# Optimization experiments

Measured on AMD Instinct MI355X. Metric: run time of the kernel, lower is better.

Reference implementation:

```python
import jax, jax.numpy as jnp
import numpy as np

B, H, W, C = 8, 64, 64, 768
NH, HD = 12, 64          # heads, head_dim
WS = 14                  # window size
MLP = 3072
EPS = 1e-6
SCALE = HD ** -0.5


def _layernorm(x, g, b):
    mu = jnp.mean(x, -1, keepdims=True)
    var = jnp.mean(jnp.square(x - mu), -1, keepdims=True)
    return (x - mu) * jax.lax.rsqrt(var + EPS) * g + b


def setup_inputs() -> dict:
    key = jax.random.key(0)
    ks = jax.random.split(key, 16)
    s = 0.02
    return {
        "hidden_states": jax.random.normal(ks[0], (B, H, W, C), jnp.float32),
        "ln1_g": jnp.ones((C,), jnp.float32),
        "ln1_b": jnp.zeros((C,), jnp.float32),
        "qkv_w": jax.random.normal(ks[1], (C, 3 * C), jnp.float32) * s,  # (in, out)
        "qkv_b": jnp.zeros((3 * C,), jnp.float32),
        "proj_w": jax.random.normal(ks[2], (C, C), jnp.float32) * s,
        "proj_b": jnp.zeros((C,), jnp.float32),
        "rel_pos_h": jax.random.normal(ks[3], (2 * WS - 1, HD), jnp.float32) * s,
        "rel_pos_w": jax.random.normal(ks[4], (2 * WS - 1, HD), jnp.float32) * s,
        "ln2_g": jnp.ones((C,), jnp.float32),
        "ln2_b": jnp.zeros((C,), jnp.float32),
        "lin1_w": jax.random.normal(ks[5], (C, MLP), jnp.float32) * s,
        "lin1_b": jnp.zeros((MLP,), jnp.float32),
        "lin2_w": jax.random.normal(ks[6], (MLP, C), jnp.float32) * s,
        "lin2_b": jnp.zeros((C,), jnp.float32),
    }


def _attention(x, qkv_w, qkv_b, proj_w, proj_b, rel_pos_h, rel_pos_w):
    # x: (Bw, WS, WS, C) windows
    Bw = x.shape[0]
    N = WS * WS
    qkv = (x.reshape(Bw, N, C) @ qkv_w + qkv_b)              # (Bw, N, 3C)
    qkv = qkv.reshape(Bw, N, 3, NH, HD).transpose(2, 0, 3, 1, 4)
    qkv = qkv.reshape(3, Bw * NH, N, HD)
    q, k, v = qkv[0], qkv[1], qkv[2]
    attn = jnp.einsum('bqd,bkd->bqk', q * SCALE, k)          # (Bw*NH, N, N)
    # decomposed relative position bias (q_size == k_size == WS, no interpolation)
    coords = jnp.arange(WS)[:, None] - jnp.arange(WS)[None, :] + (WS - 1)  # (WS, WS)
    Rh = rel_pos_h[coords]                                    # (WS, WS, HD)
    Rw = rel_pos_w[coords]
    r_q = q.reshape(Bw * NH, WS, WS, HD)
    rel_h = jnp.einsum('bhwc,hkc->bhwk', r_q, Rh)
    rel_w = jnp.einsum('bhwc,wkc->bhwk', r_q, Rw)
    attn = attn.reshape(Bw * NH, WS, WS, WS, WS)
    attn = attn + rel_h[:, :, :, :, None] + rel_w[:, :, :, None, :]
    attn = attn.reshape(Bw * NH, N, N)
    attn = jax.nn.softmax(attn.astype(jnp.float32), axis=-1).astype(q.dtype)
    out = jnp.einsum('bqk,bkd->bqd', attn, v)                 # (Bw*NH, N, HD)
    out = out.reshape(Bw, NH, WS, WS, HD).transpose(0, 2, 3, 1, 4).reshape(Bw, WS, WS, C)
    return out @ proj_w + proj_b


def _layer(x, p):
    residual = x
    h = _layernorm(x, p['ln1_g'], p['ln1_b'])
    # window partition with padding 64 -> 70
    pad_h = (WS - H % WS) % WS
    pad_w = (WS - W % WS) % WS
    h = jnp.pad(h, ((0, 0), (0, pad_h), (0, pad_w), (0, 0)))
    Hp, Wp = H + pad_h, W + pad_w
    nh, nw = Hp // WS, Wp // WS
    h = h.reshape(B, nh, WS, nw, WS, C).transpose(0, 1, 3, 2, 4, 5).reshape(-1, WS, WS, C)
    h = _attention(h, p['qkv_w'], p['qkv_b'], p['proj_w'], p['proj_b'],
                   p['rel_pos_h'], p['rel_pos_w'])
    # unpartition + crop
    h = h.reshape(B, nh, nw, WS, WS, C).transpose(0, 1, 3, 2, 4, 5).reshape(B, Hp, Wp, C)
    h = h[:, :H, :W, :]
    h = residual + h
    ln2 = _layernorm(h, p['ln2_g'], p['ln2_b'])
    mlp = jax.nn.gelu(ln2 @ p['lin1_w'] + p['lin1_b'], approximate=False) @ p['lin2_w'] + p['lin2_b']
    return h + mlp


def reference(hidden_states, ln1_g, ln1_b, qkv_w, qkv_b, proj_w, proj_b,
              rel_pos_h, rel_pos_w, ln2_g, ln2_b, lin1_w, lin1_b, lin2_w, lin2_b):
    p = dict(ln1_g=ln1_g, ln1_b=ln1_b, qkv_w=qkv_w, qkv_b=qkv_b,
             proj_w=proj_w, proj_b=proj_b, rel_pos_h=rel_pos_h, rel_pos_w=rel_pos_w,
             ln2_g=ln2_g, ln2_b=ln2_b, lin1_w=lin1_w, lin1_b=lin1_b,
             lin2_w=lin2_w, lin2_b=lin2_b)
    return _layer(hidden_states, p)
```

## Files before the change

### kernel.cpp

```cpp
#include <hip/hip_runtime.h>
#include <hip/hip_bf16.h>
#include <math.h>
#include <stdint.h>

typedef unsigned short u16;
typedef __attribute__((ext_vector_type(8))) short bf16x8;
typedef __attribute__((ext_vector_type(4))) float f32x4;

__device__ __forceinline__ float b2f(u16 u) {
  union { float f; uint32_t i; } v; v.i = ((uint32_t)u) << 16; return v.f;
}
__device__ __forceinline__ u16 f2b(float f) {
  union { float f; uint32_t i; } v; v.f = f;
  uint32_t x = v.i;
  return (u16)((x + 0x7fffu + ((x >> 16) & 1u)) >> 16);
}

__device__ __forceinline__ void gl_lds16(const u16* g, u16* l) {
  __builtin_amdgcn_global_load_lds(
      (const __attribute__((address_space(1))) void*)g,
      (__attribute__((address_space(3))) void*)l, 16, 0, 0);
}

__global__ __launch_bounds__(256)
void transpose_w(const float* __restrict__ in, u16* __restrict__ out, int K, int N) {
  __shared__ float t[32][33];
  const int x = threadIdx.x & 31;
  const int y = threadIdx.x >> 5;
  const int n0 = blockIdx.x * 32;
  const int k0 = blockIdx.y * 32;
  #pragma unroll
  for (int yy = 0; yy < 32; yy += 8)
    t[y + yy][x] = in[(size_t)(k0 + y + yy) * N + n0 + x];
  __syncthreads();
  #pragma unroll
  for (int yy = 0; yy < 32; yy += 8)
    out[(size_t)(n0 + y + yy) * K + k0 + x] = f2b(t[x][y + yy]);
}

__global__ __launch_bounds__(256)
void rel_cast(const float* __restrict__ rph, const float* __restrict__ rpw,
              u16* __restrict__ RHB, u16* __restrict__ RWB)
{
  const int i = blockIdx.x * 256 + threadIdx.x;
  if (i < 27 * 64) { RHB[i] = f2b(rph[i]); RWB[i] = f2b(rpw[i]); }
}

__global__ __launch_bounds__(256)
void ln_f32(const float* __restrict__ xin, const float* __restrict__ g,
            const float* __restrict__ b, u16* __restrict__ out)
{
  const int R = blockIdx.x * 4 + (threadIdx.x >> 6);
  const int lane = threadIdx.x & 63;
  const float* p = xin + (size_t)R * 768 + lane * 12;
  float v[12];
  float4 a0 = *(const float4*)(p);
  float4 a1 = *(const float4*)(p + 4);
  float4 a2 = *(const float4*)(p + 8);
  v[0]=a0.x; v[1]=a0.y; v[2]=a0.z;  v[3]=a0.w;
  v[4]=a1.x; v[5]=a1.y; v[6]=a1.z;  v[7]=a1.w;
  v[8]=a2.x; v[9]=a2.y; v[10]=a2.z; v[11]=a2.w;
  float sum = 0.f, sq = 0.f;
  #pragma unroll
  for (int i = 0; i < 12; ++i) { sum += v[i]; sq += v[i] * v[i]; }
  #pragma unroll
  for (int m = 1; m < 64; m <<= 1) { sum += __shfl_xor(sum, m); sq += __shfl_xor(sq, m); }
  const float mu  = sum * (1.0f / 768.0f);
  const float var = sq * (1.0f / 768.0f) - mu * mu;
  const float rs  = rsqrtf(var + 1e-6f);
  u16 o[12];
  #pragma unroll
  for (int i = 0; i < 12; ++i)
    o[i] = f2b((v[i] - mu) * rs * g[lane * 12 + i] + b[lane * 12 + i]);
  u16* q = out + (size_t)R * 768 + lane * 12;
  *(ushort4*)(q)     = make_ushort4(o[0], o[1], o[2],  o[3]);
  *(ushort4*)(q + 4) = make_ushort4(o[4], o[5], o[6],  o[7]);
  *(ushort4*)(q + 8) = make_ushort4(o[8], o[9], o[10], o[11]);
}

__global__ __launch_bounds__(256)
void qkv_padfill(const float* __restrict__ qkv_b,
                 u16* __restrict__ Qb, u16* __restrict__ Kb, u16* __restrict__ Vtb)
{
  const int R = blockIdx.x * 4 + (threadIdx.x >> 6);
  const int lane = threadIdx.x & 63;
  const int win = R / 196, n = R - win * 196;
  const int r25 = win % 25;
  const int wh = r25 / 5, ww = r25 - wh * 5;
  const int ii = n / 14,  jj = n - ii * 14;
  const int gh = wh * 14 + ii, gw = ww * 14 + jj;
  if (gh < 64 && gw < 64) return;
  #pragma unroll
  for (int head = 0; head < 12; ++head) {
    const size_t bh = (size_t)(win * 12 + head);
    Qb[(bh * 196 + n) * 64 + lane]  = f2b(qkv_b[head * 64 + lane]);
    Kb[(bh * 196 + n) * 64 + lane]  = f2b(qkv_b[768 + head * 64 + lane] * 0.125f);
    Vtb[(bh * 64 + lane) * 224 + n] = f2b(qkv_b[1536 + head * 64 + lane]);
  }
}

template<int EPI>
__global__ __launch_bounds__(256)
void gemm_bt(const u16* __restrict__ A, const u16* __restrict__ BT,
             int M, int N, int K,
             const float* __restrict__ bias,
             void* __restrict__ out0, u16* __restrict__ out1, u16* __restrict__ out2,
             const float* __restrict__ extra)
{
  __shared__ __align__(16) u16 As[128 * 32];
  __shared__ __align__(16) u16 Bs[128 * 32];
  const int tid  = threadIdx.x;
  const int lane = tid & 63;
  const int wave = tid >> 6;
  const int m0 = blockIdx.x * 128;
  const int n0 = blockIdx.y * 128;
  const int wm = (wave >> 1) << 6;
  const int wn = (wave & 1) << 6;
  const int cl = lane & 15;
  const int q4 = lane >> 4;

  f32x4 acc[4][4];
  #pragma unroll
  for (int i = 0; i < 4; ++i)
    #pragma unroll
    for (int j = 0; j < 4; ++j) acc[i][j] = f32x4{0.f, 0.f, 0.f, 0.f};

  const int sr = tid >> 2;
  const int sk = (tid & 3) << 3;
  const u16* ag0 = A  + (size_t)(m0 + sr) * K + sk;
  const u16* ag1 = A  + (size_t)(m0 + 64 + sr) * K + sk;
  const u16* bg0 = BT + (size_t)(n0 + sr) * K + sk;
  const u16* bg1 = BT + (size_t)(n0 + 64 + sr) * K + sk;

  for (int k0 = 0; k0 < K; k0 += 32) {
    __syncthreads();
    gl_lds16(ag0 + k0, &As[tid * 8]);
    gl_lds16(ag1 + k0, &As[tid * 8 + 2048]);
    gl_lds16(bg0 + k0, &Bs[tid * 8]);
    gl_lds16(bg1 + k0, &Bs[tid * 8 + 2048]);
    __syncthreads();
    bf16x8 af[4], bfv[4];
    #pragma unroll
    for (int i = 0; i < 4; ++i) af[i]  = *(const bf16x8*)&As[(wm + i * 16 + cl) * 32 + q4 * 8];
    #pragma unroll
    for (int i = 0; i < 4; ++i) bfv[i] = *(const bf16x8*)&Bs[(wn + i * 16 + cl) * 32 + q4 * 8];
    #pragma unroll
    for (int i = 0; i < 4; ++i)
      #pragma unroll
      for (int j = 0; j < 4; ++j)
        acc[i][j] = __builtin_amdgcn_mfma_f32_16x16x32_bf16(af[i], bfv[j], acc[i][j], 0, 0, 0);
  }

  #pragma unroll
  for (int mt = 0; mt < 4; ++mt) {
    #pragma unroll
    for (int nt = 0; nt < 4; ++nt) {
      const int gcol = n0 + wn + nt * 16 + cl;
      const float bval = bias[gcol];
      #pragma unroll
      for (int i = 0; i < 4; ++i) {
        const int grow = m0 + wm + mt * 16 + q4 * 4 + i;
        if (grow >= M) continue;
        float v = acc[mt][nt][i] + bval;
        if (EPI == 0) {
          const int bb = grow >> 12, rem = grow & 4095;
          const int gh = rem >> 6, gw = rem & 63;
          const int wh = gh / 14, ii = gh - wh * 14;
          const int ww = gw / 14, jj = gw - ww * 14;
          const int win = bb * 25 + wh * 5 + ww;
          const int n = ii * 14 + jj;
          const int s = (gcol >= 1536) ? 2 : (gcol >= 768 ? 1 : 0);
          const int rem2 = gcol - s * 768;
          const int head = rem2 >> 6, hd = rem2 & 63;
          const size_t bh = (size_t)(win * 12 + head);
          if (s == 0)      ((u16*)out0)[(bh * 196 + n) * 64 + hd] = f2b(v);
          else if (s == 1) out1[(bh * 196 + n) * 64 + hd] = f2b(v * 0.125f);
          else             out2[(bh * 64 + hd) * 224 + n] = f2b(v);
        } else if (EPI == 1) {
          const size_t idx = (size_t)grow * 768 + gcol;
          ((float*)out0)[idx] = v + extra[idx];
        } else {
          const float u2 = v * (1.5957691216f + 0.0713548163f * v * v);
          const float gl = v / (1.0f + __expf(-u2));
          ((u16*)out0)[(size_t)grow * 3072 + gcol] = f2b(gl);
        }
      }
    }
  }
}

__global__ __launch_bounds__(256)
void attn_kernel(const u16* __restrict__ Qb, const u16* __restrict__ Kb,
                 const u16* __restrict__ Vtb,
                 const u16* __restrict__ RHB, const u16* __restrict__ RWB,
                 u16* __restrict__ outO)
{
  __shared__ __align__(16) float Ss[32 * 201];
  __shared__ u16 MhAll[196 * 14];
  __shared__ u16 MwAll[196 * 14];
  __shared__ float Sinv[32];
  u16* Ps = (u16*)Ss;

  const int tid  = threadIdx.x;
  const int lane = tid & 63;
  const int wave = tid >> 6;
  const int cl = lane & 15;
  const int q4 = lane >> 4;
  const int bh = blockIdx.x;
  const int win = bh / 12, head = bh - win * 12;
  const int bb = win / 25, r25 = win - bb * 25;
  const int wwh = r25 / 5, www = r25 - wwh * 5;

  const u16* Qbh = Qb  + (size_t)bh * 196 * 64;
  const u16* Kbh = Kb  + (size_t)bh * 196 * 64;
  const u16* Vbh = Vtb + (size_t)bh * 64 * 224;

  for (int t = wave; t < 28; t += 4) {
    const int isW = t >= 14;
    const int grp = isW ? t - 14 : t;
    const int qrow = isW ? cl * 14 + grp : grp * 14 + cl;
    int trow = grp - cl + 13; trow = trow < 0 ? 0 : trow;
    const u16* TB = isW ? RWB : RHB;
    f32x4 acc = f32x4{0.f, 0.f, 0.f, 0.f};
    #pragma unroll
    for (int ks = 0; ks < 2; ++ks) {
      bf16x8 a  = *(const bf16x8*)(Qbh + (size_t)qrow * 64 + ks * 32 + q4 * 8);
      bf16x8 bv = *(const bf16x8*)(TB + (size_t)trow * 64 + ks * 32 + q4 * 8);
      acc = __builtin_amdgcn_mfma_f32_16x16x32_bf16(a, bv, acc, 0, 0, 0);
    }
    if (cl < 14) {
      #pragma unroll
      for (int i = 0; i < 4; ++i) {
        const int r = q4 * 4 + i;
        if (r < 14) {
          if (isW) MwAll[(r * 14 + grp) * 14 + cl] = f2b(acc[i]);
          else     MhAll[(grp * 14 + r) * 14 + cl] = f2b(acc[i]);
        }
      }
    }
  }
  __syncthreads();

  for (int c = 0; c < 7; ++c) {
    const int qbase = c * 32;
    bf16x8 afr[2][2];
    #pragma unroll
    for (int mt = 0; mt < 2; ++mt)
      #pragma unroll
      for (int ks = 0; ks < 2; ++ks)
        afr[mt][ks] = *(const bf16x8*)(Qbh + (size_t)(qbase + mt * 16 + cl) * 64 + ks * 32 + q4 * 8);

    for (int t = wave; t < 26; t += 4) {
      const int mt = t / 13, nt = t - mt * 13;
      const int col = nt * 16 + cl;
      f32x4 acc = f32x4{0.f, 0.f, 0.f, 0.f};
      #pragma unroll
      for (int ks = 0; ks < 2; ++ks) {
        bf16x8 bv = *(const bf16x8*)(Kbh + (size_t)col * 64 + ks * 32 + q4 * 8);
        acc = __builtin_amdgcn_mfma_f32_16x16x32_bf16(afr[mt][ks], bv, acc, 0, 0, 0);
      }
      if (col < 196) {
        const int kh = col / 14, kw = col - kh * 14;
        #pragma unroll
        for (int i = 0; i < 4; ++i) {
          const int r = mt * 16 + q4 * 4 + i;
          const int gq = qbase + r;
          float bias = 0.f;
          if (gq < 196) bias = b2f(MhAll[gq * 14 + kh]) + b2f(MwAll[gq * 14 + kw]);
          Ss[r * 201 + col] = acc[i] + bias;
        }
      }
    }
    __syncthreads();

    const int r = wave * 8 + (lane >> 3);
    const int s = lane & 7;
    float e[25];
    float sum = 0.f;
    #pragma unroll
    for (int k = 0; k < 25; ++k) {
      const int col = s + 8 * k;
      float ex = 0.f;
      if (col < 196) ex = __expf(fminf(Ss[r * 201 + col], 60.f));
      e[k] = ex;
      sum += ex;
    }
    sum += __shfl_xor(sum, 1);
    sum += __shfl_xor(sum, 2);
    sum += __shfl_xor(sum, 4);
    if (s == 0) Sinv[r] = 1.0f / sum;
    __syncthreads();

    #pragma unroll
    for (int k = 0; k < 25; ++k) {
      const int col = s + 8 * k;
      Ps[r * 232 + col] = (col < 196) ? f2b(e[k]) : (u16)0;
    }
    for (int z = tid; z < 384; z += 256) {
      const int rr = z / 12, m = z - rr * 12;
      *(uint32_t*)&Ps[rr * 232 + 200 + 2 * m] = 0;
    }
    __syncthreads();

    {
      const int hd = wave * 16 + cl;
      f32x4 acc0 = f32x4{0.f, 0.f, 0.f, 0.f};
      f32x4 acc1 = f32x4{0.f, 0.f, 0.f, 0.f};
      #pragma unroll
      for (int ks = 0; ks < 7; ++ks) {
        bf16x8 bv = *(const bf16x8*)(Vbh + (size_t)hd * 224 + ks * 32 + q4 * 8);
        bf16x8 a0 = *(const bf16x8*)&Ps[(cl)      * 232 + ks * 32 + q4 * 8];
        bf16x8 a1 = *(const bf16x8*)&Ps[(16 + cl) * 232 + ks * 32 + q4 * 8];
        acc0 = __builtin_amdgcn_mfma_f32_16x16x32_bf16(a0, bv, acc0, 0, 0, 0);
        acc1 = __builtin_amdgcn_mfma_f32_16x16x32_bf16(a1, bv, acc1, 0, 0, 0);
      }
      #pragma unroll
      for (int i = 0; i < 4; ++i) {
        #pragma unroll
        for (int half = 0; half < 2; ++half) {
          const int q = qbase + half * 16 + q4 * 4 + i;
          if (q < 196) {
            const float av = (half ? acc1[i] : acc0[i]) * Sinv[half * 16 + q4 * 4 + i];
            const int ii = q / 14, jj = q - ii * 14;
            const int gh = wwh * 14 + ii, gw = www * 14 + jj;
            if (gh < 64 && gw < 64)
              outO[(((size_t)bb * 64 + gh) * 64 + gw) * 768 + head * 64 + hd] = f2b(av);
          }
        }
      }
    }
    __syncthreads();
  }
}

extern "C" void kernel_launch(void* const* d_in, const int* in_sizes, int n_in,
                              void* d_out, int out_size, void* d_ws, size_t ws_size,
                              hipStream_t stream)
{
  (void)in_sizes; (void)n_in; (void)out_size; (void)ws_size;
  const float* x      = (const float*)d_in[0];
  const float* ln1_g  = (const float*)d_in[1];
  const float* ln1_b  = (const float*)d_in[2];
  const float* qkv_w  = (const float*)d_in[3];
  const float* qkv_b  = (const float*)d_in[4];
  const float* proj_w = (const float*)d_in[5];
  const float* proj_b = (const float*)d_in[6];
  const float* rph    = (const float*)d_in[7];
  const float* rpw    = (const float*)d_in[8];
  const float* ln2_g  = (const float*)d_in[9];
  const float* ln2_b  = (const float*)d_in[10];
  const float* lin1_w = (const float*)d_in[11];
  const float* lin1_b = (const float*)d_in[12];
  const float* lin2_w = (const float*)d_in[13];
  const float* lin2_b = (const float*)d_in[14];
  float* outF = (float*)d_out;

  char* ws = (char*)d_ws;
  size_t off = 0;
  auto allocB = [&](size_t bytes) -> char* {
    char* p = ws + off;
    off += (bytes + 255) & ~(size_t)255;
    return p;
  };
  u16* qkvT  = (u16*)allocB((size_t)2304 * 768 * 2);
  u16* projT = (u16*)allocB((size_t)768 * 768 * 2);
  u16* lin1T = (u16*)allocB((size_t)3072 * 768 * 2);
  u16* lin2T = (u16*)allocB((size_t)768 * 3072 * 2);
  u16* RHB   = (u16*)allocB((size_t)(27 * 64 + 64) * 2);
  u16* RWB   = (u16*)allocB((size_t)(27 * 64 + 64) * 2);
  u16* xn    = (u16*)allocB((size_t)32768 * 768 * 2);
  char* region = allocB((size_t)189235200);
  u16* Qb   = (u16*)region;
  u16* Kb   = Qb + (size_t)30105600;
  u16* Vtb  = Kb + (size_t)30105600;
  float* hbuf = (float*)region;
  u16* midQ = (u16*)(region + (size_t)100663296);

  dim3 blk(256);
  transpose_w<<<dim3(72, 24), blk, 0, stream>>>(qkv_w,  qkvT, 768, 2304);
  transpose_w<<<dim3(24, 24), blk, 0, stream>>>(proj_w, projT, 768, 768);
  transpose_w<<<dim3(96, 24), blk, 0, stream>>>(lin1_w, lin1T, 768, 3072);
  transpose_w<<<dim3(24, 96), blk, 0, stream>>>(lin2_w, lin2T, 3072, 768);
  rel_cast<<<7, blk, 0, stream>>>(rph, rpw, RHB, RWB);

  ln_f32<<<8192, blk, 0, stream>>>(x, ln1_g, ln1_b, xn);

  gemm_bt<0><<<dim3(256, 18), blk, 0, stream>>>(xn, qkvT, 32768, 2304, 768,
                                                qkv_b, Qb, Kb, Vtb, nullptr);
  qkv_padfill<<<9800, blk, 0, stream>>>(qkv_b, Qb, Kb, Vtb);

  attn_kernel<<<2400, blk, 0, stream>>>(Qb, Kb, Vtb, RHB, RWB, xn);

  gemm_bt<1><<<dim3(256, 6), blk, 0, stream>>>(xn, projT, 32768, 768, 768,
                                               proj_b, hbuf, nullptr, nullptr, x);

  ln_f32<<<8192, blk, 0, stream>>>(hbuf, ln2_g, ln2_b, xn);

  for (int pass = 0; pass < 4; ++pass) {
    const size_t ro = (size_t)pass * 8192;
    gemm_bt<2><<<dim3(64, 24), blk, 0, stream>>>(xn + ro * 768, lin1T, 8192, 3072, 768,
                                                 lin1_b, midQ, nullptr, nullptr, nullptr);
    gemm_bt<1><<<dim3(64, 6), blk, 0, stream>>>(midQ, lin2T, 8192, 768, 3072,
                                                lin2_b, outF + ro * 768, nullptr, nullptr,
                                                hbuf + ro * 768);
  }
}
```

Before: 1.564 ms.

## Remap GEMM workgroups across XCDs, use nontemporal epilogue stores, halve MLP passes

Remaps the linear workgroup id so consecutive tiles are grouped per chiplet (stride by 8). This is meant to improve L2 reuse of shared A/B tiles on the multi-XCD MI355X. The epilogue hoists the window/row index math out of the column loop and uses nontemporal loads and stores for outputs and the residual. The MLP now runs in 2 passes of 16384 rows instead of 4 of 8192, which needs a larger workspace region for the intermediate buffer and cuts the number of launches. The M bound check is dropped, which is safe only because M is a multiple of 128.

After: 1.920 ms. +22.8%, slower.

```diff
diff --git a/kernel.cpp b/kernel.cpp
--- a/kernel.cpp
+++ b/kernel.cpp
@@ -112,8 +112,15 @@
   const int tid  = threadIdx.x;
   const int lane = tid & 63;
   const int wave = tid >> 6;
-  const int m0 = blockIdx.x * 128;
-  const int n0 = blockIdx.y * 128;
+
+  const int nwg = gridDim.x * gridDim.y;
+  const int lid = blockIdx.y * gridDim.x + blockIdx.x;
+  const int nl  = (lid & 7) * (nwg >> 3) + (lid >> 3);
+  const int bx  = nl / gridDim.y;
+  const int by  = nl - bx * gridDim.y;
+  const int m0 = bx * 128;
+  const int n0 = by * 128;
+
   const int wm = (wave >> 1) << 6;
   const int wn = (wave & 1) << 6;
   const int cl = lane & 15;
@@ -153,36 +160,54 @@
 
   #pragma unroll
   for (int mt = 0; mt < 4; ++mt) {
+    int rowW[4], rowN[4];
+    if (EPI == 0) {
+      #pragma unroll
+      for (int i = 0; i < 4; ++i) {
+        const int grow = m0 + wm + mt * 16 + q4 * 4 + i;
+        const int bb = grow >> 12, rem = grow & 4095;
+        const int gh = rem >> 6, gw = rem & 63;
+        const int wh = gh / 14, ii = gh - wh * 14;
+        const int ww = gw / 14, jj = gw - ww * 14;
+        rowW[i] = (bb * 25 + wh * 5 + ww) * 12;
+        rowN[i] = ii * 14 + jj;
+      }
+    }
     #pragma unroll
     for (int nt = 0; nt < 4; ++nt) {
       const int gcol = n0 + wn + nt * 16 + cl;
       const float bval = bias[gcol];
-      #pragma unroll
-      for (int i = 0; i < 4; ++i) {
-        const int grow = m0 + wm + mt * 16 + q4 * 4 + i;
-        if (grow >= M) continue;
-        float v = acc[mt][nt][i] + bval;
-        if (EPI == 0) {
-          const int bb = grow >> 12, rem = grow & 4095;
-          const int gh = rem >> 6, gw = rem & 63;
-          const int wh = gh / 14, ii = gh - wh * 14;
-          const int ww = gw / 14, jj = gw - ww * 14;
-          const int win = bb * 25 + wh * 5 + ww;
-          const int n = ii * 14 + jj;
-          const int s = (gcol >= 1536) ? 2 : (gcol >= 768 ? 1 : 0);
-          const int rem2 = gcol - s * 768;
-          const int head = rem2 >> 6, hd = rem2 & 63;
-          const size_t bh = (size_t)(win * 12 + head);
-          if (s == 0)      ((u16*)out0)[(bh * 196 + n) * 64 + hd] = f2b(v);
-          else if (s == 1) out1[(bh * 196 + n) * 64 + hd] = f2b(v * 0.125f);
-          else             out2[(bh * 64 + hd) * 224 + n] = f2b(v);
-        } else if (EPI == 1) {
+      if (EPI == 0) {
+        const int s = (gcol >= 1536) ? 2 : (gcol >= 768 ? 1 : 0);
+        const int rem2 = gcol - s * 768;
+        const int head = rem2 >> 6, hd = rem2 & 63;
+        #pragma unroll
+        for (int i = 0; i < 4; ++i) {
+          const float v = acc[mt][nt][i] + bval;
+          const size_t bh = (size_t)(rowW[i] + head);
+          if (s == 0)
+            __builtin_nontemporal_store(f2b(v), &((u16*)out0)[(bh * 196 + rowN[i]) * 64 + hd]);
+          else if (s == 1)
+            __builtin_nontemporal_store(f2b(v * 0.125f), &out1[(bh * 196 + rowN[i]) * 64 + hd]);
+          else
+            __builtin_nontemporal_store(f2b(v), &out2[(bh * 64 + hd) * 224 + rowN[i]]);
+        }
+      } else if (EPI == 1) {
+        #pragma unroll
+        for (int i = 0; i < 4; ++i) {
+          const int grow = m0 + wm + mt * 16 + q4 * 4 + i;
           const size_t idx = (size_t)grow * 768 + gcol;
-          ((float*)out0)[idx] = v + extra[idx];
-        } else {
+          const float v = acc[mt][nt][i] + bval + __builtin_nontemporal_load(&extra[idx]);
+          __builtin_nontemporal_store(v, &((float*)out0)[idx]);
+        }
+      } else {
+        #pragma unroll
+        for (int i = 0; i < 4; ++i) {
+          const int grow = m0 + wm + mt * 16 + q4 * 4 + i;
+          const float v = acc[mt][nt][i] + bval;
           const float u2 = v * (1.5957691216f + 0.0713548163f * v * v);
           const float gl = v / (1.0f + __expf(-u2));
-          ((u16*)out0)[(size_t)grow * 3072 + gcol] = f2b(gl);
+          __builtin_nontemporal_store(f2b(gl), &((u16*)out0)[(size_t)grow * 3072 + gcol]);
         }
       }
     }
@@ -369,7 +394,7 @@
   u16* RHB   = (u16*)allocB((size_t)(27 * 64 + 64) * 2);
   u16* RWB   = (u16*)allocB((size_t)(27 * 64 + 64) * 2);
   u16* xn    = (u16*)allocB((size_t)32768 * 768 * 2);
-  char* region = allocB((size_t)189235200);
+  char* region = allocB((size_t)201326592);
   u16* Qb   = (u16*)region;
   u16* Kb   = Qb + (size_t)30105600;
   u16* Vtb  = Kb + (size_t)30105600;
@@ -396,12 +421,12 @@
 
   ln_f32<<<8192, blk, 0, stream>>>(hbuf, ln2_g, ln2_b, xn);
 
-  for (int pass = 0; pass < 4; ++pass) {
-    const size_t ro = (size_t)pass * 8192;
-    gemm_bt<2><<<dim3(64, 24), blk, 0, stream>>>(xn + ro * 768, lin1T, 8192, 3072, 768,
-                                                 lin1_b, midQ, nullptr, nullptr, nullptr);
-    gemm_bt<1><<<dim3(64, 6), blk, 0, stream>>>(midQ, lin2T, 8192, 768, 3072,
-                                                lin2_b, outF + ro * 768, nullptr, nullptr,
-                                                hbuf + ro * 768);
-  }
-}
+  for (int pass = 0; pass < 2; ++pass) {
+    const size_t ro = (size_t)pass * 16384;
+    gemm_bt<2><<<dim3(128, 24), blk, 0, stream>>>(xn + ro * 768, lin1T, 16384, 3072, 768,
+                                                  lin1_b, midQ, nullptr, nullptr, nullptr);
+    gemm_bt<1><<<dim3(128, 6), blk, 0, stream>>>(midQ, lin2T, 16384, 768, 3072,
+                                                 lin2_b, outF + ro * 768, nullptr, nullptr,
+                                                 hbuf + ro * 768);
+  }
+}
```
